# Kernel tuning notes

Measured on AMD Instinct MI355X. Metric: run time of the kernel, lower is better.

## Reference

```python
import jax, jax.numpy as jnp
import numpy as np

B, H, S, D = 4, 16, 2048, 128

def setup_inputs() -> dict:
    key = jax.random.key(0)
    kq, kk, kv = jax.random.split(key, 3)
    query = jax.random.normal(kq, (B, H, S, D), dtype=jnp.float32)
    k = jax.random.normal(kk, (B, H, S, D), dtype=jnp.float32)
    value = jax.random.normal(kv, (B, H, S, D), dtype=jnp.float32)
    attn_mask = jnp.zeros((B, H, S, S), dtype=jnp.float32)
    return {"query": query, "key": k, "value": value, "attn_mask": attn_mask}

def reference(query, key, value, attn_mask):
    # scores: [B,H,S,S]
    scale = 1.0 / jnp.sqrt(jnp.asarray(query.shape[-1], query.dtype))
    scores = jnp.einsum('bhqd,bhkd->bhqk', query, key) * scale + attn_mask
    attn = jax.nn.softmax(scores, axis=-1)
    out = jnp.einsum('bhqk,bhkd->bhqd', attn, value)
    return out
```

## Files before the change

kernel.cpp:

```cpp
#include <hip/hip_runtime.h>

#define SDIM 2048
#define DDIM 128
#define NBH  64
#define BR   128
#define BC   64
#define PSTRIDE 72

using bf16x8 = __attribute__((ext_vector_type(8))) short;
using f32x4  = __attribute__((ext_vector_type(4))) float;

static __device__ __forceinline__ short f2bf(float x) {
    unsigned u = __float_as_uint(x);
    u += 0x7fff + ((u >> 16) & 1);
    return (short)(u >> 16);
}
static __device__ __forceinline__ unsigned pack2(float a, float b) {
    return ((unsigned)(unsigned short)f2bf(a)) |
           (((unsigned)(unsigned short)f2bf(b)) << 16);
}

__global__ __launch_bounds__(256) void kconv_kernel(const float* __restrict__ K,
                                                    unsigned short* __restrict__ Kc,
                                                    unsigned* __restrict__ flag)
{
    if (flag != nullptr && blockIdx.x == 0 && threadIdx.x == 0) *flag = 0u;
    size_t i = ((size_t)blockIdx.x * 256 + threadIdx.x) * 4;
    float4 v = *(const float4*)(K + i);
    uint2 o;
    o.x = pack2(v.x, v.y);
    o.y = pack2(v.z, v.w);
    *(uint2*)(Kc + i) = o;
}

__global__ __launch_bounds__(256) void vtrans_kernel(const float* __restrict__ V,
                                                     unsigned short* __restrict__ Vt)
{
    __shared__ float t[32][33];
    const int bh = blockIdx.z;
    const int s0 = blockIdx.x * 32;
    const int d0 = blockIdx.y * 32;
    const int x = threadIdx.x & 31;
    const int y = threadIdx.x >> 5;
    const float* Vb = V + (size_t)bh * SDIM * DDIM;
    unsigned short* Vtb = Vt + (size_t)bh * SDIM * DDIM;
#pragma unroll
    for (int i = 0; i < 4; ++i) {
        int r = y + i * 8;
        t[r][x] = Vb[(size_t)(s0 + r) * DDIM + d0 + x];
    }
    __syncthreads();
#pragma unroll
    for (int i = 0; i < 4; ++i) {
        int r = y + i * 8;
        Vtb[(size_t)(d0 + r) * SDIM + s0 + x] = (unsigned short)f2bf(t[x][r]);
    }
}

__global__ __launch_bounds__(256) void maskscan_kernel(const uint4* __restrict__ M4,
                                                       unsigned* __restrict__ flag)
{
    const size_t n4 = (size_t)NBH * SDIM * SDIM / 4;
    unsigned acc = 0;
    for (size_t i = (size_t)blockIdx.x * 256 + threadIdx.x; i < n4;
         i += (size_t)gridDim.x * 256) {
        uint4 v = M4[i];
        acc |= v.x | v.y | v.z | v.w;
    }
    if (acc) *flag = 1u;
}

static __device__ __forceinline__ void load_mask(const float* __restrict__ Mb,
                                                 int q0, int wave, int quad, int n16,
                                                 int kcol, float (&mk)[2][4][4])
{
#pragma unroll
    for (int rt = 0; rt < 2; ++rt) {
        const int rowb = q0 + wave * 32 + rt * 16 + quad * 4;
        const float* mpb = Mb + (size_t)rowb * SDIM + kcol + n16;
#pragma unroll
        for (int ct = 0; ct < 4; ++ct)
#pragma unroll
            for (int r = 0; r < 4; ++r)
                mk[rt][ct][r] = mpb[(size_t)r * SDIM + ct * 16];
    }
}

template<bool MASKED>
static __device__ __forceinline__ void ktile_body(
    int k0, int q0, int wave, int quad, int n16, int lane,
    const float* __restrict__ Mb,
    const unsigned short* __restrict__ Kb, const unsigned short* __restrict__ Vb,
    unsigned short* __restrict__ PsW,
    const bf16x8 (&qf)[2][4],
    f32x4 (&acc)[2][8], float (&mrow)[2][4], float (&lrow)[2][4])
{
    const f32x4 zero4 = {0.f, 0.f, 0.f, 0.f};

    bf16x8 kfr[4][4];
#pragma unroll
    for (int dt = 0; dt < 4; ++dt)
#pragma unroll
        for (int ct = 0; ct < 4; ++ct)
            kfr[dt][ct] = *(const bf16x8*)(Kb + (size_t)(k0 + ct * 16 + n16) * DDIM + dt * 32 + quad * 8);

    float mk[2][4][4];
    if constexpr (MASKED)
        load_mask(Mb, q0, wave, quad, n16, k0, mk);

    f32x4 s[2][4];
#pragma unroll
    for (int rt = 0; rt < 2; ++rt)
#pragma unroll
        for (int ct = 0; ct < 4; ++ct) s[rt][ct] = zero4;
#pragma unroll
    for (int dt = 0; dt < 4; ++dt) {
#pragma unroll
        for (int ct = 0; ct < 4; ++ct) {
            s[0][ct] = __builtin_amdgcn_mfma_f32_16x16x32_bf16(qf[0][dt], kfr[dt][ct], s[0][ct], 0, 0, 0);
            s[1][ct] = __builtin_amdgcn_mfma_f32_16x16x32_bf16(qf[1][dt], kfr[dt][ct], s[1][ct], 0, 0, 0);
        }
    }

    if constexpr (MASKED) {
#pragma unroll
        for (int rt = 0; rt < 2; ++rt)
#pragma unroll
            for (int ct = 0; ct < 4; ++ct)
#pragma unroll
                for (int r = 0; r < 4; ++r)
                    s[rt][ct][r] += mk[rt][ct][r];
    }

    float mx[2][4];
#pragma unroll
    for (int rt = 0; rt < 2; ++rt)
#pragma unroll
        for (int r = 0; r < 4; ++r)
            mx[rt][r] = fmaxf(fmaxf(s[rt][0][r], s[rt][1][r]),
                              fmaxf(s[rt][2][r], s[rt][3][r]));
#pragma unroll
    for (int st = 1; st <= 8; st <<= 1)
#pragma unroll
        for (int rt = 0; rt < 2; ++rt)
#pragma unroll
            for (int r = 0; r < 4; ++r)
                mx[rt][r] = fmaxf(mx[rt][r], __shfl_xor(mx[rt][r], st));

    int anynew = 0;
#pragma unroll
    for (int rt = 0; rt < 2; ++rt)
#pragma unroll
        for (int r = 0; r < 4; ++r)
            anynew |= (mx[rt][r] > mrow[rt][r]) ? 1 : 0;
    if (__ballot(anynew) != 0ull) {
#pragma unroll
        for (int rt = 0; rt < 2; ++rt)
#pragma unroll
            for (int r = 0; r < 4; ++r) {
                float mnew = fmaxf(mrow[rt][r], mx[rt][r]);
                float al = exp2f((mrow[rt][r] - mnew) * 1.44269504f);
                mrow[rt][r] = mnew;
                lrow[rt][r] *= al;
#pragma unroll
                for (int nt = 0; nt < 8; ++nt) acc[rt][nt][r] *= al;
            }
    }

    float rs[2][4];
#pragma unroll
    for (int rt = 0; rt < 2; ++rt)
#pragma unroll
        for (int r = 0; r < 4; ++r) {
            float t = 0.f;
#pragma unroll
            for (int ct = 0; ct < 4; ++ct) {
                float pv = exp2f((s[rt][ct][r] - mrow[rt][r]) * 1.44269504f);
                s[rt][ct][r] = pv;
                t += pv;
            }
            rs[rt][r] = t;
        }
#pragma unroll
    for (int st = 1; st <= 8; st <<= 1)
#pragma unroll
        for (int rt = 0; rt < 2; ++rt)
#pragma unroll
            for (int r = 0; r < 4; ++r)
                rs[rt][r] += __shfl_xor(rs[rt][r], st);
#pragma unroll
    for (int rt = 0; rt < 2; ++rt)
#pragma unroll
        for (int r = 0; r < 4; ++r)
            lrow[rt][r] += rs[rt][r];

#pragma unroll
    for (int rt = 0; rt < 2; ++rt)
#pragma unroll
        for (int ct = 0; ct < 4; ++ct)
#pragma unroll
            for (int r = 0; r < 4; ++r)
                PsW[(rt * 16 + (lane >> 4) * 4 + r) * PSTRIDE + ct * 16 + n16] =
                    (unsigned short)f2bf(s[rt][ct][r]);

    bf16x8 pa[2][2];
#pragma unroll
    for (int rt = 0; rt < 2; ++rt)
#pragma unroll
        for (int kt = 0; kt < 2; ++kt)
            pa[rt][kt] = *(const bf16x8*)(&PsW[(rt * 16 + n16) * PSTRIDE + kt * 32 + quad * 8]);

#pragma unroll
    for (int nt = 0; nt < 8; ++nt) {
#pragma unroll
        for (int kt = 0; kt < 2; ++kt) {
            bf16x8 vf = *(const bf16x8*)(Vb + (size_t)(nt * 16 + n16) * SDIM + k0 + kt * 32 + quad * 8);
            acc[0][nt] = __builtin_amdgcn_mfma_f32_16x16x32_bf16(pa[0][kt], vf, acc[0][nt], 0, 0, 0);
            acc[1][nt] = __builtin_amdgcn_mfma_f32_16x16x32_bf16(pa[1][kt], vf, acc[1][nt], 0, 0, 0);
        }
    }
}

__global__ __launch_bounds__(256, 2) void fattn_kernel(
    const float* __restrict__ Q, const float* __restrict__ M,
    const unsigned short* __restrict__ Kc, const unsigned short* __restrict__ Vt,
    const unsigned* __restrict__ flag,
    float* __restrict__ O)
{
    const int flat = blockIdx.x;
    const int slot = flat >> 3;
    const int bh   = (flat & 7) * 8 + (slot >> 4);
    const int qt   = slot & 15;

    const int tid  = threadIdx.x;
    const int wave = tid >> 6;
    const int lane = tid & 63;
    const int quad = lane >> 4;
    const int n16  = lane & 15;
    const int q0   = qt * BR;

    const float* Qb = Q + (size_t)bh * SDIM * DDIM;
    const float* Mb = M + (size_t)bh * SDIM * SDIM;
    const unsigned short* Kb = Kc + (size_t)bh * SDIM * DDIM;
    const unsigned short* Vb = Vt + (size_t)bh * SDIM * DDIM;
    float* Ob = O + (size_t)bh * SDIM * DDIM;

    const bool masked = (flag == nullptr) || (*flag != 0u);

    __shared__ __align__(16) unsigned short Ps[4][32 * PSTRIDE];
    unsigned short* PsW = Ps[wave];

    const float scale = 0.08838834764831845f;
    bf16x8 qf[2][4];
#pragma unroll
    for (int rt = 0; rt < 2; ++rt) {
        int row = q0 + wave * 32 + rt * 16 + n16;
        const float* qp = Qb + (size_t)row * DDIM + quad * 8;
#pragma unroll
        for (int dt = 0; dt < 4; ++dt) {
            const float* p = qp + dt * 32;
            float4 a = *(const float4*)p;
            float4 b = *(const float4*)(p + 4);
            bf16x8 f;
            f[0] = f2bf(a.x * scale); f[1] = f2bf(a.y * scale);
            f[2] = f2bf(a.z * scale); f[3] = f2bf(a.w * scale);
            f[4] = f2bf(b.x * scale); f[5] = f2bf(b.y * scale);
            f[6] = f2bf(b.z * scale); f[7] = f2bf(b.w * scale);
            qf[rt][dt] = f;
        }
    }

    f32x4 acc[2][8];
    const f32x4 zero4 = {0.f, 0.f, 0.f, 0.f};
#pragma unroll
    for (int rt = 0; rt < 2; ++rt)
#pragma unroll
        for (int nt = 0; nt < 8; ++nt) acc[rt][nt] = zero4;
    float mrow[2][4], lrow[2][4];
#pragma unroll
    for (int rt = 0; rt < 2; ++rt)
#pragma unroll
        for (int r = 0; r < 4; ++r) { mrow[rt][r] = -1e30f; lrow[rt][r] = 0.f; }

    if (!masked) {
#pragma unroll 1
        for (int k0 = 0; k0 < SDIM; k0 += BC)
            ktile_body<false>(k0, q0, wave, quad, n16, lane, Mb, Kb, Vb, PsW,
                              qf, acc, mrow, lrow);
    } else {
#pragma unroll 1
        for (int k0 = 0; k0 < SDIM; k0 += BC)
            ktile_body<true>(k0, q0, wave, quad, n16, lane, Mb, Kb, Vb, PsW,
                             qf, acc, mrow, lrow);
    }

#pragma unroll
    for (int rt = 0; rt < 2; ++rt) {
#pragma unroll
        for (int r = 0; r < 4; ++r) {
            float inv = 1.0f / lrow[rt][r];
            int row = q0 + wave * 32 + rt * 16 + quad * 4 + r;
            float* op = Ob + (size_t)row * DDIM + n16;
#pragma unroll
            for (int nt = 0; nt < 8; ++nt)
                op[nt * 16] = acc[rt][nt][r] * inv;
        }
    }
}

extern "C" void kernel_launch(void* const* d_in, const int* in_sizes, int n_in,
                              void* d_out, int out_size, void* d_ws, size_t ws_size,
                              hipStream_t stream) {
    const float* Q = (const float*)d_in[0];
    const float* K = (const float*)d_in[1];
    const float* V = (const float*)d_in[2];
    const float* M = (const float*)d_in[3];
    float* O = (float*)d_out;

    const size_t nElem = (size_t)NBH * SDIM * DDIM;
    unsigned short* Kc = (unsigned short*)d_ws;
    unsigned short* Vt = Kc + nElem;

    const size_t kvBytes = 2 * nElem * sizeof(unsigned short);
    unsigned* flag = (ws_size >= kvBytes + sizeof(unsigned))
                   ? (unsigned*)((char*)d_ws + kvBytes) : nullptr;

    kconv_kernel<<<dim3(nElem / (256 * 4)), 256, 0, stream>>>(K, Kc, flag);
    vtrans_kernel<<<dim3(SDIM / 32, DDIM / 32, NBH), 256, 0, stream>>>(V, Vt);
    if (flag != nullptr)
        maskscan_kernel<<<dim3(2048), 256, 0, stream>>>((const uint4*)M, flag);

    fattn_kernel<<<dim3((SDIM / BR) * NBH), 256, 0, stream>>>(Q, M, Kc, Vt, flag, O);
}
```

Baseline: 1.938 ms.

## Stage K and V tiles in swizzled LDS via direct global-to-LDS loads

Each k-tile's K and V slices are now loaded cooperatively by all four waves into shared memory with global_load_lds, using an XOR swizzle, instead of each wave reading its own fragments from global memory. The intent is to cut redundant global/L2 traffic, since every wave previously fetched the same K/V data. The MFMA blocks are also wrapped in s_setprio raises. The cost is two __syncthreads per tile, a single non-double-buffered stage with no overlap, and extra LDS use that may affect the two-blocks-per-CU occupancy target.

After: 1.767 ms. -8.8%, faster.

```diff
diff --git a/kernel.cpp b/kernel.cpp
--- a/kernel.cpp
+++ b/kernel.cpp
@@ -9,6 +9,9 @@
 
 using bf16x8 = __attribute__((ext_vector_type(8))) short;
 using f32x4  = __attribute__((ext_vector_type(4))) float;
+
+typedef const __attribute__((address_space(1))) void* gvp;
+typedef __attribute__((address_space(3))) void* lvp;
 
 static __device__ __forceinline__ short f2bf(float x) {
     unsigned u = __float_as_uint(x);
@@ -91,23 +94,38 @@
     int k0, int q0, int wave, int quad, int n16, int lane,
     const float* __restrict__ Mb,
     const unsigned short* __restrict__ Kb, const unsigned short* __restrict__ Vb,
+    char* __restrict__ Kl, char* __restrict__ Vl,
     unsigned short* __restrict__ PsW,
     const bf16x8 (&qf)[2][4],
     f32x4 (&acc)[2][8], float (&mrow)[2][4], float (&lrow)[2][4])
 {
     const f32x4 zero4 = {0.f, 0.f, 0.f, 0.f};
 
-    bf16x8 kfr[4][4];
-#pragma unroll
-    for (int dt = 0; dt < 4; ++dt)
-#pragma unroll
-        for (int ct = 0; ct < 4; ++ct)
-            kfr[dt][ct] = *(const bf16x8*)(Kb + (size_t)(k0 + ct * 16 + n16) * DDIM + dt * 32 + quad * 8);
+#pragma unroll
+    for (int j = 0; j < 4; ++j) {
+        const int row = wave * 16 + j * 4 + quad;
+        const int src = (n16 * 16) ^ ((row & 7) << 4);
+        const char* gp = (const char*)(Kb + (size_t)(k0 + row) * DDIM) + src;
+        char* lp = Kl + wave * 4096 + j * 1024;
+        __builtin_amdgcn_global_load_lds((gvp)gp, (lvp)lp, 16, 0, 0);
+    }
+#pragma unroll
+    for (int j = 0; j < 4; ++j) {
+        const int row = wave * 32 + j * 8 + (lane >> 3);
+        const int src = ((lane & 7) * 16) ^ ((row & 7) << 4);
+        const char* gp = (const char*)(Vb + (size_t)row * SDIM + k0) + src;
+        char* lp = Vl + wave * 4096 + j * 1024;
+        __builtin_amdgcn_global_load_lds((gvp)gp, (lvp)lp, 16, 0, 0);
+    }
 
     float mk[2][4][4];
     if constexpr (MASKED)
         load_mask(Mb, q0, wave, quad, n16, k0, mk);
 
+    __syncthreads();
+
+    const int swzr = (n16 & 7) << 4;
+
     f32x4 s[2][4];
 #pragma unroll
     for (int rt = 0; rt < 2; ++rt)
@@ -115,11 +133,18 @@
         for (int ct = 0; ct < 4; ++ct) s[rt][ct] = zero4;
 #pragma unroll
     for (int dt = 0; dt < 4; ++dt) {
+        bf16x8 kf[4];
+#pragma unroll
+        for (int ct = 0; ct < 4; ++ct)
+            kf[ct] = *(const bf16x8*)(Kl + (ct * 16 + n16) * 256 +
+                                      ((dt * 64 + quad * 16) ^ swzr));
+        __builtin_amdgcn_s_setprio(1);
 #pragma unroll
         for (int ct = 0; ct < 4; ++ct) {
-            s[0][ct] = __builtin_amdgcn_mfma_f32_16x16x32_bf16(qf[0][dt], kfr[dt][ct], s[0][ct], 0, 0, 0);
-            s[1][ct] = __builtin_amdgcn_mfma_f32_16x16x32_bf16(qf[1][dt], kfr[dt][ct], s[1][ct], 0, 0, 0);
-        }
+            s[0][ct] = __builtin_amdgcn_mfma_f32_16x16x32_bf16(qf[0][dt], kf[ct], s[0][ct], 0, 0, 0);
+            s[1][ct] = __builtin_amdgcn_mfma_f32_16x16x32_bf16(qf[1][dt], kf[ct], s[1][ct], 0, 0, 0);
+        }
+        __builtin_amdgcn_s_setprio(0);
     }
 
     if constexpr (MASKED) {
@@ -212,12 +237,18 @@
 
 #pragma unroll
     for (int nt = 0; nt < 8; ++nt) {
+        bf16x8 vf[2];
+#pragma unroll
+        for (int kt = 0; kt < 2; ++kt)
+            vf[kt] = *(const bf16x8*)(Vl + (nt * 16 + n16) * 128 +
+                                      ((kt * 64 + quad * 16) ^ swzr));
+        __builtin_amdgcn_s_setprio(1);
 #pragma unroll
         for (int kt = 0; kt < 2; ++kt) {
-            bf16x8 vf = *(const bf16x8*)(Vb + (size_t)(nt * 16 + n16) * SDIM + k0 + kt * 32 + quad * 8);
-            acc[0][nt] = __builtin_amdgcn_mfma_f32_16x16x32_bf16(pa[0][kt], vf, acc[0][nt], 0, 0, 0);
-            acc[1][nt] = __builtin_amdgcn_mfma_f32_16x16x32_bf16(pa[1][kt], vf, acc[1][nt], 0, 0, 0);
-        }
+            acc[0][nt] = __builtin_amdgcn_mfma_f32_16x16x32_bf16(pa[0][kt], vf[kt], acc[0][nt], 0, 0, 0);
+            acc[1][nt] = __builtin_amdgcn_mfma_f32_16x16x32_bf16(pa[1][kt], vf[kt], acc[1][nt], 0, 0, 0);
+        }
+        __builtin_amdgcn_s_setprio(0);
     }
 }
 
@@ -247,6 +278,8 @@
 
     const bool masked = (flag == nullptr) || (*flag != 0u);
 
+    __shared__ __align__(16) char Kl[64 * 256];
+    __shared__ __align__(16) char Vl[128 * 128];
     __shared__ __align__(16) unsigned short Ps[4][32 * PSTRIDE];
     unsigned short* PsW = Ps[wave];
 
@@ -284,14 +317,18 @@
 
     if (!masked) {
 #pragma unroll 1
-        for (int k0 = 0; k0 < SDIM; k0 += BC)
-            ktile_body<false>(k0, q0, wave, quad, n16, lane, Mb, Kb, Vb, PsW,
-                              qf, acc, mrow, lrow);
+        for (int k0 = 0; k0 < SDIM; k0 += BC) {
+            __syncthreads();
+            ktile_body<false>(k0, q0, wave, quad, n16, lane, Mb, Kb, Vb,
+                              Kl, Vl, PsW, qf, acc, mrow, lrow);
+        }
     } else {
 #pragma unroll 1
-        for (int k0 = 0; k0 < SDIM; k0 += BC)
-            ktile_body<true>(k0, q0, wave, quad, n16, lane, Mb, Kb, Vb, PsW,
-                             qf, acc, mrow, lrow);
+        for (int k0 = 0; k0 < SDIM; k0 += BC) {
+            __syncthreads();
+            ktile_body<true>(k0, q0, wave, quad, n16, lane, Mb, Kb, Vb,
+                             Kl, Vl, PsW, qf, acc, mrow, lrow);
+        }
     }
 
 #pragma unroll
```
